# Performance work log

Measured on AMD Instinct MI355X. Metric: run time of the kernel, lower is better.

## Reference

```python
import jax, jax.numpy as jnp
import numpy as np
from jax import lax

THRESHOLD = 0.9


def _conv(x, w, b, stride):
    # x: [B,C,H,W], w: [O,I,3,3] (OIHW)
    y = lax.conv_general_dilated(x, w, (stride, stride), 'SAME',
                                 dimension_numbers=('NCHW', 'OIHW', 'NCHW'))
    return y + b[None, :, None, None]


def _expert(x, w1, b1, w2, b2, wf, bf):
    h = jax.nn.relu(_conv(x, w1, b1, 2))   # [B,64,112,112]
    h = jax.nn.relu(_conv(h, w2, b2, 2))   # [B,128,56,56]
    g = h.mean(axis=(2, 3))                # [B,128] global average pool
    return g @ wf + bf                     # [B,2] logits


def setup_inputs() -> dict:
    key = jax.random.key(0)
    ks = jax.random.split(key, 13)
    f32 = jnp.float32
    def rn(k, shape, scale):
        return jax.random.normal(k, shape, dtype=f32) * scale
    return {
        'x':    rn(ks[0], (64, 3, 224, 224), 1.0),
        't_w1': rn(ks[1], (64, 3, 3, 3),   0.2),
        't_b1': jnp.zeros((64,), f32),
        't_w2': rn(ks[2], (128, 64, 3, 3), 0.05),
        't_b2': jnp.zeros((128,), f32),
        't_wf': rn(ks[3], (128, 2),        0.1),
        't_bf': jnp.zeros((2,), f32),
        'f_w1': rn(ks[4], (64, 3, 3, 3),   0.2),
        'f_b1': jnp.zeros((64,), f32),
        'f_w2': rn(ks[5], (128, 64, 3, 3), 0.05),
        'f_b2': jnp.zeros((128,), f32),
        'f_wf': rn(ks[6], (128, 2),        0.1),
        'f_bf': jnp.zeros((2,), f32),
    }


def reference(x, t_w1, t_b1, t_w2, t_b2, t_wf, t_bf,
              f_w1, f_b1, f_w2, f_b2, f_wf, f_bf):
    t_logits = _expert(x, t_w1, t_b1, t_w2, t_b2, t_wf, t_bf)   # [B,2]
    t_conf = jax.nn.softmax(t_logits, axis=1).max(axis=1)        # [B]
    use_texture2 = t_conf <= THRESHOLD                           # [B] bool
    # jit-friendly dense evaluation of the second expert; the where-mask
    # reproduces the original gather/scatter blend exactly (values and grads).
    f_logits = _expert(x, f_w1, f_b1, f_w2, f_b2, f_wf, f_bf)   # [B,2]
    output = jnp.where(use_texture2[:, None],
                       0.7 * t_logits + 0.3 * f_logits,
                       t_logits)
    freq_usage = use_texture2.astype(jnp.float32).mean()
    return (output, freq_usage)
```

## Files before the change

### kernel.cpp

```cpp
#include <hip/hip_runtime.h>
#include <hip/hip_fp16.h>
#include <math.h>


#define W2B_OFF   0ull
#define W1F_OFF   294912ull
#define G_OFF     303104ull
#define H1_OFF    368640ull
#define H1E_US    52301824ull
#define H1B_US    817216ull
#define WS_NEED   (H1_OFF + 2ull*H1E_US*2ull + 4096ull)

typedef __attribute__((ext_vector_type(8))) short bf16x8;
typedef __attribute__((ext_vector_type(8))) _Float16 half8;
typedef __attribute__((ext_vector_type(4))) float f32x4;

__device__ inline ushort f2h(float v) {
  __half h = __float2half(v);
  return *(ushort*)&h;
}

__global__ __launch_bounds__(256) void prep_new(
    const float* __restrict__ w2_t, const float* __restrict__ w2_f,
    const float* __restrict__ w1_t, const float* __restrict__ w1_f,
    char* __restrict__ ws) {
  int idx = blockIdx.x * 256 + threadIdx.x;
  ushort* w2frag = (ushort*)(ws + W2B_OFF);
  ushort* w1frag = (ushort*)(ws + W1F_OFF);
  if (idx < 147456) {
    int j    = idx & 7;
    int lane = (idx >> 3) & 63;
    int t2   = idx >> 9;
    int kc   = t2 % 18;
    int t3   = t2 / 18;
    int octile = t3 & 7;
    int e    = t3 >> 3;
    int oc = octile * 16 + (lane & 15);
    int kk = kc * 32 + (lane >> 4) * 8 + j;
    int kh = kk / 192, r2 = kk - kh * 192, kw = r2 >> 6, slot = r2 & 63;
    int icp = ((slot >> 2) & 3) * 16 + ((slot >> 4) & 3) * 4 + (slot & 3);
    const float* src = e ? w2_f : w2_t;
    w2frag[idx] = f2h(src[((oc * 64 + icp) * 3 + kh) * 3 + kw]);
  } else if (idx < 147456 + 4096) {
    int i2   = idx - 147456;
    int j    = i2 & 7;
    int lane = (i2 >> 3) & 63;
    int m    = (i2 >> 9) & 3;
    int e    = (i2 >> 11) & 1;
    int oc = m * 16 + (lane & 15);
    int kk = (lane >> 4) * 8 + j;
    const float* src = e ? w1_f : w1_t;
    w1frag[i2] = f2h((kk < 27) ? src[oc * 27 + kk] : 0.f);
  } else if (idx < 147456 + 4096 + 16384) {
    ((float*)(ws + G_OFF))[idx - 151552] = 0.f;
  }
}

__global__ __launch_bounds__(256) void conv1_mfma(
    const float* __restrict__ x,
    const ushort* __restrict__ w1f_all,
    const float* __restrict__ b1_t, const float* __restrict__ b1_f,
    ushort* __restrict__ h1_all)
{
  const int gR  = blockIdx.x;
  const int b   = blockIdx.y;
  const int e   = blockIdx.z;
  const int tid = threadIdx.x;
  const int w    = tid >> 6;
  const int lane = tid & 63;
  const int q    = lane >> 4;
  const int n    = lane & 15;

  ushort* h1b = h1_all + (size_t)e * H1E_US + (size_t)b * H1B_US;
  const float* b1 = e ? b1_f : b1_t;

  constexpr int CW = 233;
  __shared__ unsigned int xs[3 * 9 * CW];

  const float* xb = x + (size_t)b * 150528;
  const int xr0 = 8 * gR;
  for (int i = tid; i < 1512; i += 256) {
    int ic  = i / 504;
    int rem = i - ic * 504;
    int r   = rem / 56;
    int u   = rem - r * 56;
    int xr  = xr0 + r;
    float4 p = make_float4(0.f, 0.f, 0.f, 0.f);
    if (xr < 224) p = *(const float4*)(xb + (ic * 224 + xr) * 224 + 4 * u);
    int base = (ic * 9 + r) * CW + 4 * u;
    xs[base + 0] = (unsigned int)f2h(p.x);
    xs[base + 1] = (unsigned int)f2h(p.y);
    xs[base + 2] = (unsigned int)f2h(p.z);
    xs[base + 3] = (unsigned int)f2h(p.w);
  }
  if (tid < 27) xs[tid * CW + 224] = 0;

  h1b[((size_t)((4 * gR + (tid >> 6)) * 113 + 112)) * 64 + (tid & 63)] = 0;
  if (gR == 0) {
    unsigned int* z = (unsigned int*)&h1b[(size_t)112 * 113 * 64];
    for (int i = tid; i < 3616; i += 256) z[i] = 0;
  }

  half8 wf[4];
#pragma unroll
  for (int m = 0; m < 4; ++m)
    wf[m] = *(const half8*)&w1f_all[(((size_t)(e * 4 + m)) * 64 + lane) * 8];
  float4 bv[4];
#pragma unroll
  for (int m = 0; m < 4; ++m)
    bv[m] = *(const float4*)&b1[m * 16 + 4 * q];

  int off[8];
#pragma unroll
  for (int j = 0; j < 8; ++j) {
    int kk = q * 8 + j;
    if (kk < 27) {
      int ic = kk / 9;
      int r9 = kk - ic * 9;
      int kh = r9 / 3;
      int kw = r9 - kh * 3;
      off[j] = (ic * 9 + kh) * CW + kw;
    } else {
      off[j] = -1;
    }
  }

  __syncthreads();

  const int row   = 4 * gR + w;
  const int rbase = (2 * w) * CW;

  for (int nt = 0; nt < 7; ++nt) {
    const int c = nt * 16 + n;
    const int base = rbase + 2 * c;
    unsigned int g[8];
#pragma unroll
    for (int j = 0; j < 8; ++j)
      g[j] = (off[j] >= 0) ? xs[base + off[j]] : 0u;
    union { half8 h; unsigned int u[4]; } bh;
#pragma unroll
    for (int p = 0; p < 4; ++p)
      bh.u[p] = (g[2 * p] & 0xffffu) | (g[2 * p + 1] << 16);
    f32x4 acc[4];
#pragma unroll
    for (int m = 0; m < 4; ++m) acc[m] = (f32x4){0.f, 0.f, 0.f, 0.f};
#pragma unroll
    for (int m = 0; m < 4; ++m)
      acc[m] = __builtin_amdgcn_mfma_f32_16x16x32_f16(wf[m], bh.h, acc[m], 0, 0, 0);
    size_t po = ((size_t)(row * 113 + c)) * 64 + q * 16;
    union { ushort us[16]; uint4 v4[2]; } pk;
#pragma unroll
    for (int m = 0; m < 4; ++m) {
      pk.us[m * 4 + 0] = f2h(fmaxf(acc[m][0] + bv[m].x, 0.f));
      pk.us[m * 4 + 1] = f2h(fmaxf(acc[m][1] + bv[m].y, 0.f));
      pk.us[m * 4 + 2] = f2h(fmaxf(acc[m][2] + bv[m].z, 0.f));
      pk.us[m * 4 + 3] = f2h(fmaxf(acc[m][3] + bv[m].w, 0.f));
    }
    *(uint4*)&h1b[po]     = pk.v4[0];
    *(uint4*)&h1b[po + 8] = pk.v4[1];
  }
}

__global__ __launch_bounds__(256, 2) void conv2_mfma(
    const ushort* __restrict__ h1_all,
    const ushort* __restrict__ w2frag,
    const float* __restrict__ b2_t, const float* __restrict__ b2_f,
    float* __restrict__ g)
{
  const int T = blockIdx.x;
  const int b = blockIdx.y;
  const int e = blockIdx.z;
  const int tid  = threadIdx.x;
  const int w    = tid >> 6;
  const int lane = tid & 63;
  const ushort* h1b = h1_all + (size_t)e * H1E_US + (size_t)b * H1B_US;
  const float* b2 = e ? b2_f : b2_t;

  __shared__ ushort hs[5 * 113 * 64];

  const int q   = lane >> 4;
  const int n   = lane & 15;
  const int pxl = lane & 7;
  const int rl  = (lane >> 3) & 1;

  half8 afr[2][18];
#pragma unroll
  for (int mt = 0; mt < 2; ++mt)
#pragma unroll
    for (int kc = 0; kc < 18; ++kc)
      afr[mt][kc] = *(const half8*)
          &w2frag[((size_t)((e * 8 + 2 * w + mt) * 18 + kc)) * 512 + lane * 8];

#pragma unroll
  for (int half = 0; half < 2; ++half) {
    bf16x8 tmp[9];
    int dst[9];
    bool ok[9];
#pragma unroll
    for (int k = 0; k < 9; ++k) {
      int s = tid + (half * 9 + k) * 256;
      ok[k] = (s < 4520);
      int r = s / 904;
      int rem = s - 904 * r;
      int hx = rem >> 3, gq = rem & 7;
      if (ok[k])
        tmp[k] = *(const bf16x8*)&h1b[((size_t)((4 * T + r) * 113 + hx)) * 64 + 8 * gq];
      dst[k] = (r * 113 + hx) * 64 + 8 * (gq ^ (hx & 7));
    }
#pragma unroll
    for (int k = 0; k < 9; ++k)
      if (ok[k]) *(bf16x8*)&hs[dst[k]] = tmp[k];
  }
  __syncthreads();

  f32x4 acc[2][7];
#pragma unroll
  for (int mt = 0; mt < 2; ++mt)
#pragma unroll
    for (int nt = 0; nt < 7; ++nt) acc[mt][nt] = (f32x4){0.f, 0.f, 0.f, 0.f};

#pragma unroll
  for (int kh = 0; kh < 3; ++kh) {
    const int rbase = (kh + 2 * rl) * 113 * 64;
#pragma unroll
    for (int kw = 0; kw < 3; ++kw) {
#pragma unroll
      for (int icc = 0; icc < 2; ++icc) {
        const int kc = kh * 6 + kw * 2 + icc;
        const int gsw = 8 * ((icc * 4 + q) ^ ((2 * pxl + kw) & 7));
        half8 bf[7];
#pragma unroll
        for (int nt = 0; nt < 7; ++nt) {
          int hx = 2 * (8 * nt + pxl) + kw;
          bf[nt] = *(const half8*)&hs[rbase + hx * 64 + gsw];
        }
#pragma unroll
        for (int mt = 0; mt < 2; ++mt) {
#pragma unroll
          for (int nt = 0; nt < 7; ++nt)
            acc[mt][nt] = __builtin_amdgcn_mfma_f32_16x16x32_f16(
                afr[mt][kc], bf[nt], acc[mt][nt], 0, 0, 0);
        }
      }
    }
  }

#pragma unroll
  for (int mt = 0; mt < 2; ++mt) {
#pragma unroll
    for (int reg = 0; reg < 4; ++reg) {
      const int oc = 32 * w + 16 * mt + 4 * q + reg;
      const float bias = b2[oc];
      float s = 0.f;
#pragma unroll
      for (int nt = 0; nt < 7; ++nt) s += fmaxf(acc[mt][nt][reg] + bias, 0.f);
      s += __shfl_xor(s, 1);
      s += __shfl_xor(s, 2);
      s += __shfl_xor(s, 4);
      s += __shfl_xor(s, 8);
      if (n == 0) atomicAdd(&g[((size_t)e * 64 + b) * 128 + oc], s);
    }
  }
}

__global__ __launch_bounds__(256) void finale(
    const float* __restrict__ g,
    const float* __restrict__ t_wf, const float* __restrict__ t_bf,
    const float* __restrict__ f_wf, const float* __restrict__ f_bf,
    float* __restrict__ out)
{
  const int tid = threadIdx.x;
  const int b = tid >> 2;
  const int j = tid & 3;
  const float inv = 1.0f / 3136.0f;
  const float* gt = g + b * 128;
  const float* gf = g + (64 + b) * 128;
  float lt0 = 0.f, lt1 = 0.f, lf0 = 0.f, lf1 = 0.f;
  const int k0 = j * 32;
#pragma unroll 8
  for (int k = k0; k < k0 + 32; ++k) {
    float vt = gt[k] * inv;
    float vf = gf[k] * inv;
    lt0 = fmaf(vt, t_wf[2 * k],     lt0);
    lt1 = fmaf(vt, t_wf[2 * k + 1], lt1);
    lf0 = fmaf(vf, f_wf[2 * k],     lf0);
    lf1 = fmaf(vf, f_wf[2 * k + 1], lf1);
  }
  lt0 += __shfl_xor(lt0, 1); lt0 += __shfl_xor(lt0, 2);
  lt1 += __shfl_xor(lt1, 1); lt1 += __shfl_xor(lt1, 2);
  lf0 += __shfl_xor(lf0, 1); lf0 += __shfl_xor(lf0, 2);
  lf1 += __shfl_xor(lf1, 1); lf1 += __shfl_xor(lf1, 2);
  __shared__ int cnt[64];
  if (j == 0) {
    lt0 += t_bf[0]; lt1 += t_bf[1];
    lf0 += f_bf[0]; lf1 += f_bf[1];
    float m  = fmaxf(lt0, lt1);
    float e0 = expf(lt0 - m), e1 = expf(lt1 - m);
    float conf = fmaxf(e0, e1) / (e0 + e1);
    bool use2 = (conf <= 0.9f);
    out[2 * b]     = use2 ? 0.7f * lt0 + 0.3f * lf0 : lt0;
    out[2 * b + 1] = use2 ? 0.7f * lt1 + 0.3f * lf1 : lt1;
    cnt[b] = use2 ? 1 : 0;
  }
  __syncthreads();
  if (tid == 0) {
    int s = 0;
#pragma unroll
    for (int i = 0; i < 64; ++i) s += cnt[i];
    out[128] = (float)s * (1.0f / 64.0f);
  }
}

__global__ __launch_bounds__(256) void transpose_w2(
    const float* __restrict__ w2_t, const float* __restrict__ w2_f,
    float* __restrict__ w2t) {
  int idx = blockIdx.x * 256 + threadIdx.x;
  int e = idx / 73728;
  int r = idx - e * 73728;
  int k = r >> 7, oc = r & 127;
  const float* src = e ? w2_f : w2_t;
  w2t[idx] = src[oc * 576 + k];
}

__global__ __launch_bounds__(256, 3) void fused_expert(
    const float* __restrict__ x,
    const float* __restrict__ w1_t, const float* __restrict__ b1_t,
    const float* __restrict__ b2_t,
    const float* __restrict__ w1_f, const float* __restrict__ b1_f,
    const float* __restrict__ b2_f,
    const float* __restrict__ w2t_all, float* __restrict__ g)
{
  const int tile = blockIdx.x, b = blockIdx.y, e = blockIdx.z;
  const int ty = tile >> 1, tx = tile & 1;
  const float* w1  = e ? w1_f : w1_t;
  const float* b1  = e ? b1_f : b1_t;
  const float* b2  = e ? b2_f : b2_t;
  const float* w2t = w2t_all + e * 73728;
  __shared__ float x_s[3 * 19 * 116];
  __shared__ float h1_s[8 * 9 * 58];
  __shared__ float w1_s[1728];
  const int tid = threadIdx.x;
  {
    const float* xb = x + (size_t)b * 150528;
    const int xr0 = ty * 16, xc0 = tx * 112;
    for (int idx = tid; idx < 3 * 19 * 116; idx += 256) {
      int ic = idx / (19 * 116);
      int rem = idx - ic * (19 * 116);
      int r = rem / 116, cc = rem - r * 116;
      int xr = xr0 + r, xc = xc0 + cc;
      float v = 0.f;
      if (xr < 224 && xc < 224 && cc < 115) v = xb[(ic * 224 + xr) * 224 + xc];
      x_s[idx] = v;
    }
    for (int idx = tid; idx < 1728; idx += 256) w1_s[idx] = w1[idx];
  }
  const int ocg = tid >> 4, posg = tid & 15;
  int pbase[7];
#pragma unroll
  for (int j = 0; j < 7; ++j) {
    int p = posg + 16 * j, py = p / 28, px = p - py * 28;
    pbase[j] = py * 2 * 58 + px * 2;
  }
  float acc[7][8];
#pragma unroll
  for (int j = 0; j < 7; ++j)
#pragma unroll
    for (int i = 0; i < 8; ++i) acc[j][i] = 0.f;
  const int hc_l = tid >> 5, l32 = tid & 31;
  for (int c = 0; c < 8; ++c) {
    __syncthreads();
    {
      const int hc = c * 8 + hc_l;
      const float bias = b1[hc];
      float wr[27];
#pragma unroll
      for (int qq = 0; qq < 27; ++qq) wr[qq] = w1_s[hc * 27 + qq];
      for (int p = l32; p < 513; p += 32) {
        int hy = p / 57, hx = p - hy * 57;
        float a = bias;
#pragma unroll
        for (int ic = 0; ic < 3; ++ic)
#pragma unroll
          for (int kh = 0; kh < 3; ++kh) {
            const float* row = &x_s[ic * (19 * 116) + (2 * hy + kh) * 116 + 2 * hx];
            a = fmaf(row[0], wr[ic * 9 + kh * 3 + 0], a);
            a = fmaf(row[1], wr[ic * 9 + kh * 3 + 1], a);
            a = fmaf(row[2], wr[ic * 9 + kh * 3 + 2], a);
          }
        float v = fmaxf(a, 0.f);
        int hy_g = ty * 8 + hy, hx_g = tx * 56 + hx;
        if (hy_g >= 112 || hx_g >= 112) v = 0.f;
        h1_s[hc_l * 522 + hy * 58 + hx] = v;
      }
    }
    __syncthreads();
    for (int ic_l = 0; ic_l < 8; ++ic_l) {
#pragma unroll
      for (int kh = 0; kh < 3; ++kh)
#pragma unroll
        for (int kw = 0; kw < 3; ++kw) {
          const int k = (c * 8 + ic_l) * 9 + kh * 3 + kw;
          const float4 wA = *(const float4*)(w2t + k * 128 + ocg * 8);
          const float4 wB = *(const float4*)(w2t + k * 128 + ocg * 8 + 4);
          const float* hp = &h1_s[ic_l * 522 + kh * 58 + kw];
#pragma unroll
          for (int j = 0; j < 7; ++j) {
            float h = hp[pbase[j]];
            acc[j][0] = fmaf(wA.x, h, acc[j][0]);
            acc[j][1] = fmaf(wA.y, h, acc[j][1]);
            acc[j][2] = fmaf(wA.z, h, acc[j][2]);
            acc[j][3] = fmaf(wA.w, h, acc[j][3]);
            acc[j][4] = fmaf(wB.x, h, acc[j][4]);
            acc[j][5] = fmaf(wB.y, h, acc[j][5]);
            acc[j][6] = fmaf(wB.z, h, acc[j][6]);
            acc[j][7] = fmaf(wB.w, h, acc[j][7]);
          }
        }
    }
  }
  __syncthreads();
  float* red = x_s;
#pragma unroll
  for (int i = 0; i < 8; ++i) {
    float bb = b2[ocg * 8 + i];
    float t = 0.f;
#pragma unroll
    for (int j = 0; j < 7; ++j) t += fmaxf(acc[j][i] + bb, 0.f);
    red[posg * 129 + ocg * 8 + i] = t;
  }
  __syncthreads();
  if (tid < 128) {
    float t = 0.f;
#pragma unroll
    for (int pg = 0; pg < 16; ++pg) t += red[pg * 129 + tid];
    atomicAdd(&g[(e * 64 + b) * 128 + tid], t);
  }
}

__global__ __launch_bounds__(64) void finale_old(
    const float* __restrict__ g,
    const float* __restrict__ t_wf, const float* __restrict__ t_bf,
    const float* __restrict__ f_wf, const float* __restrict__ f_bf,
    float* __restrict__ out)
{
  const int b = threadIdx.x;
  const float inv = 1.0f / 3136.0f;
  const float* gt = g + b * 128;
  const float* gf = g + (64 + b) * 128;
  float lt0 = t_bf[0], lt1 = t_bf[1];
  float lf0 = f_bf[0], lf1 = f_bf[1];
  for (int k = 0; k < 128; ++k) {
    float vt = gt[k] * inv;
    float vf = gf[k] * inv;
    lt0 = fmaf(vt, t_wf[2 * k],     lt0);
    lt1 = fmaf(vt, t_wf[2 * k + 1], lt1);
    lf0 = fmaf(vf, f_wf[2 * k],     lf0);
    lf1 = fmaf(vf, f_wf[2 * k + 1], lf1);
  }
  float m  = fmaxf(lt0, lt1);
  float e0 = expf(lt0 - m), e1 = expf(lt1 - m);
  float conf = fmaxf(e0, e1) / (e0 + e1);
  bool use2 = (conf <= 0.9f);
  out[2 * b]     = use2 ? 0.7f * lt0 + 0.3f * lf0 : lt0;
  out[2 * b + 1] = use2 ? 0.7f * lt1 + 0.3f * lf1 : lt1;
  unsigned long long mask = __ballot(use2);
  if (b == 0) out[128] = (float)__popcll(mask) * (1.0f / 64.0f);
}

extern "C" void kernel_launch(void* const* d_in, const int* in_sizes, int n_in,
                              void* d_out, int out_size, void* d_ws, size_t ws_size,
                              hipStream_t stream) {
  const float* x    = (const float*)d_in[0];
  const float* t_w1 = (const float*)d_in[1];
  const float* t_b1 = (const float*)d_in[2];
  const float* t_w2 = (const float*)d_in[3];
  const float* t_b2 = (const float*)d_in[4];
  const float* t_wf = (const float*)d_in[5];
  const float* t_bf = (const float*)d_in[6];
  const float* f_w1 = (const float*)d_in[7];
  const float* f_b1 = (const float*)d_in[8];
  const float* f_w2 = (const float*)d_in[9];
  const float* f_b2 = (const float*)d_in[10];
  const float* f_wf = (const float*)d_in[11];
  const float* f_bf = (const float*)d_in[12];
  float* out = (float*)d_out;
  char* ws = (char*)d_ws;

  if (ws_size >= WS_NEED) {
    float*  gbuf   = (float*)(ws + G_OFF);
    ushort* h1     = (ushort*)(ws + H1_OFF);
    ushort* w2frag = (ushort*)(ws + W2B_OFF);
    ushort* w1f    = (ushort*)(ws + W1F_OFF);
    prep_new<<<656, 256, 0, stream>>>(t_w2, f_w2, t_w1, f_w1, ws);
    conv1_mfma<<<dim3(28, 64, 2), 256, 0, stream>>>(x, w1f, t_b1, f_b1, h1);
    conv2_mfma<<<dim3(28, 64, 2), 256, 0, stream>>>(h1, w2frag, t_b2, f_b2, gbuf);
    finale<<<1, 256, 0, stream>>>(gbuf, t_wf, t_bf, f_wf, f_bf, out);
  } else {
    float* w2t = (float*)ws;
    float* g2  = (float*)(ws + 589824);
    hipMemsetAsync(g2, 0, 2 * 64 * 128 * sizeof(float), stream);
    transpose_w2<<<576, 256, 0, stream>>>(t_w2, f_w2, w2t);
    fused_expert<<<dim3(28, 64, 2), 256, 0, stream>>>(
        x, t_w1, t_b1, t_b2, f_w1, f_b1, f_b2, w2t, g2);
    finale_old<<<1, 64, 0, stream>>>(g2, t_wf, t_bf, f_wf, f_bf, out);
  }
}
```

Measured before the change: 243.2 us.

## Fold weight prep into conv1 and finale into conv2 via last-block counter

Removes the separate prep kernel by having conv1 blocks with gR==0 convert slices of conv2 weights, gR==1 blocks zero the pooled-sum buffer, and every block build its conv1 weight fragments directly from fp32 weights. Removes the finale kernel by having the last conv2 block, found through an atomic counter, compute logits, the gating blend and the usage fraction. This cuts launches from four to two, in exchange for extra per-block weight conversion work and a global atomic and fence at the end of each conv2 block.

```diff
diff --git a/kernel.cpp b/kernel.cpp
--- a/kernel.cpp
+++ b/kernel.cpp
@@ -4,12 +4,12 @@
 
 
 #define W2B_OFF   0ull
-#define W1F_OFF   294912ull
 #define G_OFF     303104ull
 #define H1_OFF    368640ull
 #define H1E_US    52301824ull
 #define H1B_US    817216ull
-#define WS_NEED   (H1_OFF + 2ull*H1E_US*2ull + 4096ull)
+#define CNT_OFF   (H1_OFF + 2ull*H1E_US*2ull)
+#define WS_NEED   (CNT_OFF + 4096ull)
 
 typedef __attribute__((ext_vector_type(8))) short bf16x8;
 typedef __attribute__((ext_vector_type(8))) _Float16 half8;
@@ -20,47 +20,12 @@
   return *(ushort*)&h;
 }
 
-__global__ __launch_bounds__(256) void prep_new(
-    const float* __restrict__ w2_t, const float* __restrict__ w2_f,
-    const float* __restrict__ w1_t, const float* __restrict__ w1_f,
-    char* __restrict__ ws) {
-  int idx = blockIdx.x * 256 + threadIdx.x;
-  ushort* w2frag = (ushort*)(ws + W2B_OFF);
-  ushort* w1frag = (ushort*)(ws + W1F_OFF);
-  if (idx < 147456) {
-    int j    = idx & 7;
-    int lane = (idx >> 3) & 63;
-    int t2   = idx >> 9;
-    int kc   = t2 % 18;
-    int t3   = t2 / 18;
-    int octile = t3 & 7;
-    int e    = t3 >> 3;
-    int oc = octile * 16 + (lane & 15);
-    int kk = kc * 32 + (lane >> 4) * 8 + j;
-    int kh = kk / 192, r2 = kk - kh * 192, kw = r2 >> 6, slot = r2 & 63;
-    int icp = ((slot >> 2) & 3) * 16 + ((slot >> 4) & 3) * 4 + (slot & 3);
-    const float* src = e ? w2_f : w2_t;
-    w2frag[idx] = f2h(src[((oc * 64 + icp) * 3 + kh) * 3 + kw]);
-  } else if (idx < 147456 + 4096) {
-    int i2   = idx - 147456;
-    int j    = i2 & 7;
-    int lane = (i2 >> 3) & 63;
-    int m    = (i2 >> 9) & 3;
-    int e    = (i2 >> 11) & 1;
-    int oc = m * 16 + (lane & 15);
-    int kk = (lane >> 4) * 8 + j;
-    const float* src = e ? w1_f : w1_t;
-    w1frag[i2] = f2h((kk < 27) ? src[oc * 27 + kk] : 0.f);
-  } else if (idx < 147456 + 4096 + 16384) {
-    ((float*)(ws + G_OFF))[idx - 151552] = 0.f;
-  }
-}
-
 __global__ __launch_bounds__(256) void conv1_mfma(
     const float* __restrict__ x,
-    const ushort* __restrict__ w1f_all,
+    const float* __restrict__ w1_t, const float* __restrict__ w1_f,
     const float* __restrict__ b1_t, const float* __restrict__ b1_f,
-    ushort* __restrict__ h1_all)
+    const float* __restrict__ w2_t, const float* __restrict__ w2_f,
+    char* __restrict__ ws)
 {
   const int gR  = blockIdx.x;
   const int b   = blockIdx.y;
@@ -71,11 +36,39 @@
   const int q    = lane >> 4;
   const int n    = lane & 15;
 
+  ushort* h1_all = (ushort*)(ws + H1_OFF);
   ushort* h1b = h1_all + (size_t)e * H1E_US + (size_t)b * H1B_US;
   const float* b1 = e ? b1_f : b1_t;
 
   constexpr int CW = 233;
   __shared__ unsigned int xs[3 * 9 * CW];
+
+  if (gR == 0) {
+    ushort* w2frag = (ushort*)(ws + W2B_OFF);
+    const int base = (e * 64 + b) * 1152;
+    for (int i = tid; i < 1152; i += 256) {
+      int idx   = base + i;
+      int j     = idx & 7;
+      int lane2 = (idx >> 3) & 63;
+      int t2    = idx >> 9;
+      int kc    = t2 % 18;
+      int t3    = t2 / 18;
+      int octile = t3 & 7;
+      int ee    = t3 >> 3;
+      int oc = octile * 16 + (lane2 & 15);
+      int kk = kc * 32 + (lane2 >> 4) * 8 + j;
+      int kh = kk / 192, r2k = kk - kh * 192, kw = r2k >> 6, slot = r2k & 63;
+      int icp = ((slot >> 2) & 3) * 16 + ((slot >> 4) & 3) * 4 + (slot & 3);
+      const float* src = ee ? w2_f : w2_t;
+      w2frag[idx] = f2h(src[((oc * 64 + icp) * 3 + kh) * 3 + kw]);
+    }
+  } else if (gR == 1) {
+    float* gz = (float*)(ws + G_OFF);
+    const int base = (e * 64 + b) * 128;
+    for (int i = tid; i < 128; i += 256) gz[base + i] = 0.f;
+  } else if (gR == 2 && b == 0 && e == 0 && tid == 0) {
+    *(unsigned int*)(ws + CNT_OFF) = 0u;
+  }
 
   const float* xb = x + (size_t)b * 150528;
   const int xr0 = 8 * gR;
@@ -101,10 +94,18 @@
     for (int i = tid; i < 3616; i += 256) z[i] = 0;
   }
 
+  const float* w1s = e ? w1_f : w1_t;
   half8 wf[4];
 #pragma unroll
-  for (int m = 0; m < 4; ++m)
-    wf[m] = *(const half8*)&w1f_all[(((size_t)(e * 4 + m)) * 64 + lane) * 8];
+  for (int m = 0; m < 4; ++m) {
+    union { half8 h; ushort us[8]; } u;
+#pragma unroll
+    for (int j = 0; j < 8; ++j) {
+      int kk = q * 8 + j;
+      u.us[j] = f2h((kk < 27) ? w1s[(m * 16 + n) * 27 + kk] : 0.f);
+    }
+    wf[m] = u.h;
+  }
   float4 bv[4];
 #pragma unroll
   for (int m = 0; m < 4; ++m)
@@ -165,7 +166,10 @@
     const ushort* __restrict__ h1_all,
     const ushort* __restrict__ w2frag,
     const float* __restrict__ b2_t, const float* __restrict__ b2_f,
-    float* __restrict__ g)
+    const float* __restrict__ t_wf, const float* __restrict__ t_bf,
+    const float* __restrict__ f_wf, const float* __restrict__ f_bf,
+    float* __restrict__ g, unsigned int* __restrict__ cnt,
+    float* __restrict__ out)
 {
   const int T = blockIdx.x;
   const int b = blockIdx.y;
@@ -177,6 +181,7 @@
   const float* b2 = e ? b2_f : b2_t;
 
   __shared__ ushort hs[5 * 113 * 64];
+  __shared__ unsigned int last_flag;
 
   const int q   = lane >> 4;
   const int n   = lane & 15;
@@ -261,53 +266,52 @@
       if (n == 0) atomicAdd(&g[((size_t)e * 64 + b) * 128 + oc], s);
     }
   }
-}
-
-__global__ __launch_bounds__(256) void finale(
-    const float* __restrict__ g,
-    const float* __restrict__ t_wf, const float* __restrict__ t_bf,
-    const float* __restrict__ f_wf, const float* __restrict__ f_bf,
-    float* __restrict__ out)
-{
-  const int tid = threadIdx.x;
-  const int b = tid >> 2;
-  const int j = tid & 3;
-  const float inv = 1.0f / 3136.0f;
-  const float* gt = g + b * 128;
-  const float* gf = g + (64 + b) * 128;
-  float lt0 = 0.f, lt1 = 0.f, lf0 = 0.f, lf1 = 0.f;
-  const int k0 = j * 32;
-#pragma unroll 8
-  for (int k = k0; k < k0 + 32; ++k) {
-    float vt = gt[k] * inv;
-    float vf = gf[k] * inv;
-    lt0 = fmaf(vt, t_wf[2 * k],     lt0);
-    lt1 = fmaf(vt, t_wf[2 * k + 1], lt1);
-    lf0 = fmaf(vf, f_wf[2 * k],     lf0);
-    lf1 = fmaf(vf, f_wf[2 * k + 1], lf1);
-  }
-  lt0 += __shfl_xor(lt0, 1); lt0 += __shfl_xor(lt0, 2);
-  lt1 += __shfl_xor(lt1, 1); lt1 += __shfl_xor(lt1, 2);
-  lf0 += __shfl_xor(lf0, 1); lf0 += __shfl_xor(lf0, 2);
-  lf1 += __shfl_xor(lf1, 1); lf1 += __shfl_xor(lf1, 2);
-  __shared__ int cnt[64];
-  if (j == 0) {
-    lt0 += t_bf[0]; lt1 += t_bf[1];
-    lf0 += f_bf[0]; lf1 += f_bf[1];
-    float m  = fmaxf(lt0, lt1);
-    float e0 = expf(lt0 - m), e1 = expf(lt1 - m);
-    float conf = fmaxf(e0, e1) / (e0 + e1);
-    bool use2 = (conf <= 0.9f);
-    out[2 * b]     = use2 ? 0.7f * lt0 + 0.3f * lf0 : lt0;
-    out[2 * b + 1] = use2 ? 0.7f * lt1 + 0.3f * lf1 : lt1;
-    cnt[b] = use2 ? 1 : 0;
-  }
+
+  __threadfence();
   __syncthreads();
-  if (tid == 0) {
-    int s = 0;
-#pragma unroll
-    for (int i = 0; i < 64; ++i) s += cnt[i];
-    out[128] = (float)s * (1.0f / 64.0f);
+  if (tid == 0)
+    last_flag = (atomicAdd(cnt, 1u) == 28u * 64u * 2u - 1u) ? 1u : 0u;
+  __syncthreads();
+  if (last_flag) {
+    __threadfence();
+    const int bb = tid >> 2;
+    const int jj = tid & 3;
+    const float inv = 1.0f / 3136.0f;
+    float* gt = g + bb * 128;
+    float* gf = g + (64 + bb) * 128;
+    float lt0 = 0.f, lt1 = 0.f, lf0 = 0.f, lf1 = 0.f;
+    const int k0 = jj * 32;
+    for (int k = k0; k < k0 + 32; ++k) {
+      float vt = atomicAdd(&gt[k], 0.f) * inv;
+      float vf = atomicAdd(&gf[k], 0.f) * inv;
+      lt0 = fmaf(vt, t_wf[2 * k],     lt0);
+      lt1 = fmaf(vt, t_wf[2 * k + 1], lt1);
+      lf0 = fmaf(vf, f_wf[2 * k],     lf0);
+      lf1 = fmaf(vf, f_wf[2 * k + 1], lf1);
+    }
+    lt0 += __shfl_xor(lt0, 1); lt0 += __shfl_xor(lt0, 2);
+    lt1 += __shfl_xor(lt1, 1); lt1 += __shfl_xor(lt1, 2);
+    lf0 += __shfl_xor(lf0, 1); lf0 += __shfl_xor(lf0, 2);
+    lf1 += __shfl_xor(lf1, 1); lf1 += __shfl_xor(lf1, 2);
+    int* cs = (int*)hs;
+    if (jj == 0) {
+      lt0 += t_bf[0]; lt1 += t_bf[1];
+      lf0 += f_bf[0]; lf1 += f_bf[1];
+      float m  = fmaxf(lt0, lt1);
+      float e0 = expf(lt0 - m), e1 = expf(lt1 - m);
+      float conf = fmaxf(e0, e1) / (e0 + e1);
+      bool use2 = (conf <= 0.9f);
+      out[2 * bb]     = use2 ? 0.7f * lt0 + 0.3f * lf0 : lt0;
+      out[2 * bb + 1] = use2 ? 0.7f * lt1 + 0.3f * lf1 : lt1;
+      cs[bb] = use2 ? 1 : 0;
+    }
+    __syncthreads();
+    if (tid == 0) {
+      int s = 0;
+#pragma unroll
+      for (int i = 0; i < 64; ++i) s += cs[i];
+      out[128] = (float)s * (1.0f / 64.0f);
+    }
   }
 }
 
@@ -490,11 +494,11 @@
     float*  gbuf   = (float*)(ws + G_OFF);
     ushort* h1     = (ushort*)(ws + H1_OFF);
     ushort* w2frag = (ushort*)(ws + W2B_OFF);
-    ushort* w1f    = (ushort*)(ws + W1F_OFF);
-    prep_new<<<656, 256, 0, stream>>>(t_w2, f_w2, t_w1, f_w1, ws);
-    conv1_mfma<<<dim3(28, 64, 2), 256, 0, stream>>>(x, w1f, t_b1, f_b1, h1);
-    conv2_mfma<<<dim3(28, 64, 2), 256, 0, stream>>>(h1, w2frag, t_b2, f_b2, gbuf);
-    finale<<<1, 256, 0, stream>>>(gbuf, t_wf, t_bf, f_wf, f_bf, out);
+    unsigned int* cnt = (unsigned int*)(ws + CNT_OFF);
+    conv1_mfma<<<dim3(28, 64, 2), 256, 0, stream>>>(
+        x, t_w1, f_w1, t_b1, f_b1, t_w2, f_w2, ws);
+    conv2_mfma<<<dim3(28, 64, 2), 256, 0, stream>>>(
+        h1, w2frag, t_b2, f_b2, t_wf, t_bf, f_wf, f_bf, gbuf, cnt, out);
   } else {
     float* w2t = (float*)ws;
     float* g2  = (float*)(ws + 589824);
```

Result: slower. 621.7 us (+155.6%).
